# Optimization experiments

Measured on AMD Instinct MI355X. Metric: run time of the kernel, lower is better.

Reference implementation:

```python
import jax, jax.numpy as jnp
import numpy as np


def setup_inputs() -> dict:
    key = jax.random.key(0)
    ks = jax.random.split(key, 7)
    B, C, H, W = 8, 1024, 64, 64
    heads, head_dim, red = 8, 128, 8
    s = 1.0 / np.sqrt(head_dim)
    return {
        "x": jax.random.normal(ks[0], (B, C, H, W), jnp.float32),
        "Wq": jax.random.normal(ks[1], (heads, red, head_dim), jnp.float32) * s,
        "bq": jax.random.normal(ks[2], (heads, red), jnp.float32) * s,
        "Wk": jax.random.normal(ks[3], (heads, red, head_dim), jnp.float32) * s,
        "bk": jax.random.normal(ks[4], (heads, red), jnp.float32) * s,
        "Wv": jax.random.normal(ks[5], (heads, head_dim, head_dim), jnp.float32) * s,
        "bv": jax.random.normal(ks[6], (heads, head_dim), jnp.float32) * s,
    }


def reference(x, Wq, bq, Wk, bk, Wv, bv):
    B, C, H, W = x.shape
    heads, red, d = Wq.shape  # d = head_dim
    # (B, heads, head_dim, HW)
    xh = x.reshape(B, heads, d, H * W)
    # per-head spatial average pool: (B, heads, head_dim)
    avg = jnp.mean(xh, axis=-1)
    # torch Linear: y = x @ W.T + b, applied per head
    q = jnp.einsum("bhds,hrd->bhsr", xh, Wq) + bq[None, :, None, :]   # (B,H,S,r)
    k = jnp.einsum("bhd,hrd->bhr", avg, Wk) + bk[None]                 # (B,H,r)
    v = jnp.einsum("bhd,hed->bhe", avg, Wv) + bv[None]                 # (B,H,d)
    # single-key attention; softmax over the spatial dim (torch dim=1)
    scores = jnp.einsum("bhsr,bhr->bhs", q, k)                          # (B,H,S)
    attn = jax.nn.softmax(scores, axis=-1)
    out = jnp.einsum("bhs,bhe->bhes", attn, v)                          # (B,H,d,S)
    return out.reshape(B, C, H, W)
```

## Files before the change

### kernel.cpp

```cpp
#include <hip/hip_runtime.h>
#include <math.h>

#define SDIM 4096
#define DDIM 128
#define RED 8
#define BATCH 8
#define BH 64
#define CH 1024

typedef float vfloat4 __attribute__((ext_vector_type(4)));

#define WS_AVG  0
#define WS_VV   32768
#define WS_ATT  40960
#define WS_QRP  303104
#define QRP_DG  2097152

__inline__ __device__ float wave_reduce_sum(float v) {
#pragma unroll
    for (int o = 32; o > 0; o >>= 1) v += __shfl_down(v, o, 64);
    return v;
}
__inline__ __device__ float wave_reduce_max(float v) {
#pragma unroll
    for (int o = 32; o > 0; o >>= 1) v = fmaxf(v, __shfl_down(v, o, 64));
    return v;
}

__global__ __launch_bounds__(256, 4) void k_qr(
        const float* __restrict__ x, const float* __restrict__ Wq,
        float* __restrict__ ws) {
    const int blk = blockIdx.x;
    const int dg = blk & 3, chunk = (blk >> 2) & 3, bh = blk >> 4;
    const int h = bh & 7;
    const int t = threadIdx.x;
    const int wave = t >> 6, lane = t & 63;
    const int r8 = lane >> 3, seg = lane & 7;

    __shared__ float wqt[32 * 8];
    __shared__ float sxy[4][8][65];
    __shared__ float fpart[4][4][8][9];

    wqt[t] = Wq[(h * RED + (t & 7)) * DDIM + dg * 32 + (t >> 3)];
    __syncthreads();

    const int s0 = chunk * 1024 + t * 4;
    const float* xb = x + (size_t)(bh * DDIM + dg * 32) * SDIM + s0;
    vfloat4 accq[RED];
#pragma unroll
    for (int r = 0; r < RED; ++r) accq[r] = (vfloat4)0.f;

#pragma unroll
    for (int g = 0; g < 4; ++g) {
#pragma unroll
        for (int j = 0; j < 8; ++j) {
            const int dl = g * 8 + j;
            const vfloat4 xv = *(const vfloat4*)(xb + (size_t)dl * SDIM);
            const float4 wa = *(const float4*)&wqt[dl * 8];
            const float4 wb = *(const float4*)&wqt[dl * 8 + 4];
            accq[0] += xv * wa.x;
            accq[1] += xv * wa.y;
            accq[2] += xv * wa.z;
            accq[3] += xv * wa.w;
            accq[4] += xv * wb.x;
            accq[5] += xv * wb.y;
            accq[6] += xv * wb.z;
            accq[7] += xv * wb.w;
            sxy[wave][j][lane] = xv[0] + xv[1] + xv[2] + xv[3];
        }
        float ps = 0.f;
#pragma unroll
        for (int j = 0; j < 8; ++j) ps += sxy[wave][r8][seg * 8 + j];
        fpart[wave][g][r8][seg] = ps;
    }

    float* qb = ws + WS_QRP + (size_t)dg * QRP_DG + (size_t)(bh * RED) * SDIM + s0;
#pragma unroll
    for (int r = 0; r < RED; ++r)
        *(vfloat4*)(qb + (size_t)r * SDIM) = accq[r];

    __syncthreads();
    if (t < 32) {
        const int g = t >> 3, rr = t & 7;
        float a = 0.f;
#pragma unroll
        for (int w = 0; w < 4; ++w)
#pragma unroll
            for (int s2 = 0; s2 < 8; ++s2)
                a += fpart[w][g][rr][s2];
        ws[WS_AVG + chunk * 8192 + bh * DDIM + dg * 32 + t] = a;
    }
}

__global__ __launch_bounds__(256) void k_head(
        const float* __restrict__ bq, const float* __restrict__ Wk,
        const float* __restrict__ bk, const float* __restrict__ Wv,
        const float* __restrict__ bv, float* __restrict__ ws) {
    const int bh = blockIdx.x;
    const int h = bh & 7;
    const int t = threadIdx.x;
    const int wave = t >> 6, lane = t & 63;

    __shared__ float avgs[DDIM], kk[RED], bqs[RED];
    __shared__ float smax[4], ssum[4];
    __shared__ float cc;

    if (t < DDIM) {
        float a = 0.f;
#pragma unroll
        for (int c = 0; c < 4; ++c) a += ws[WS_AVG + c * 8192 + bh * DDIM + t];
        avgs[t] = a * (1.0f / SDIM);
    }
    __syncthreads();
    if (t < RED) {
        const float* wkr = Wk + (h * RED + t) * DDIM;
        float a = 0.f;
#pragma unroll 8
        for (int d = 0; d < DDIM; ++d) a += wkr[d] * avgs[d];
        kk[t] = a + bk[h * RED + t];
        bqs[t] = bq[h * RED + t];
    }
    if (t < DDIM) {
        const float* wvr = Wv + (h * DDIM + t) * DDIM;
        float a = 0.f;
#pragma unroll 8
        for (int d = 0; d < DDIM; ++d) a += wvr[d] * avgs[d];
        ws[WS_VV + bh * DDIM + t] = a + bv[h * DDIM + t];
    }
    __syncthreads();
    if (t == 0) {
        float a = 0.f;
#pragma unroll
        for (int r = 0; r < RED; ++r) a += bqs[r] * kk[r];
        cc = a;
    }
    __syncthreads();

    float4 vals[4];
    float m = -1e30f;
#pragma unroll
    for (int p = 0; p < 4; ++p) {
        float4 a;
        a.x = cc; a.y = cc; a.z = cc; a.w = cc;
#pragma unroll
        for (int r = 0; r < RED; ++r) {
            const size_t base = WS_QRP + (size_t)(bh * RED + r) * SDIM + (t + 256 * p) * 4;
            float4 q0 = *(const float4*)(ws + base);
            float4 q1 = *(const float4*)(ws + base + QRP_DG);
            float4 q2 = *(const float4*)(ws + base + 2 * (size_t)QRP_DG);
            float4 q3 = *(const float4*)(ws + base + 3 * (size_t)QRP_DG);
            const float kr = kk[r];
            a.x += (q0.x + q1.x + q2.x + q3.x) * kr;
            a.y += (q0.y + q1.y + q2.y + q3.y) * kr;
            a.z += (q0.z + q1.z + q2.z + q3.z) * kr;
            a.w += (q0.w + q1.w + q2.w + q3.w) * kr;
        }
        vals[p] = a;
        m = fmaxf(m, fmaxf(fmaxf(a.x, a.y), fmaxf(a.z, a.w)));
    }
    m = wave_reduce_max(m);
    if (lane == 0) smax[wave] = m;
    __syncthreads();
    const float gm = fmaxf(fmaxf(smax[0], smax[1]), fmaxf(smax[2], smax[3]));
    float sum = 0.f;
#pragma unroll
    for (int p = 0; p < 4; ++p) {
        vals[p].x = expf(vals[p].x - gm);
        vals[p].y = expf(vals[p].y - gm);
        vals[p].z = expf(vals[p].z - gm);
        vals[p].w = expf(vals[p].w - gm);
        sum += vals[p].x + vals[p].y + vals[p].z + vals[p].w;
    }
    sum = wave_reduce_sum(sum);
    if (lane == 0) ssum[wave] = sum;
    __syncthreads();
    const float inv = 1.0f / (ssum[0] + ssum[1] + ssum[2] + ssum[3]);
    float4* att4 = (float4*)(ws + WS_ATT + (size_t)bh * SDIM);
#pragma unroll
    for (int p = 0; p < 4; ++p) {
        float4 o;
        o.x = vals[p].x * inv; o.y = vals[p].y * inv;
        o.z = vals[p].z * inv; o.w = vals[p].w * inv;
        att4[t + 256 * p] = o;
    }
}

__global__ __launch_bounds__(256) void k_wr(const float* __restrict__ ws,
                                            float* __restrict__ out) {
    const int blk = blockIdx.x;
    const int bh = blk >> 4, chunk = blk & 15;
    const int t = threadIdx.x;
    const int wave = t >> 6, lane = t & 63;

    __shared__ float vvs[DDIM];
    if (t < DDIM) vvs[t] = ws[WS_VV + bh * DDIM + t];

    const vfloat4 a4 =
        ((const vfloat4*)(ws + WS_ATT))[bh * 1024 + chunk * 64 + lane];
    __syncthreads();

    vfloat4* ob = (vfloat4*)out + (size_t)(bh * DDIM) * 1024 + chunk * 64 + lane;
#pragma unroll
    for (int i = 0; i < 32; ++i) {
        const int e = wave * 32 + i;
        vfloat4 o = a4 * vvs[e];
        __builtin_nontemporal_store(o, ob + (size_t)e * 1024);
    }
}

extern "C" void kernel_launch(void* const* d_in, const int* in_sizes, int n_in,
                              void* d_out, int out_size, void* d_ws, size_t ws_size,
                              hipStream_t stream) {
    const float* x  = (const float*)d_in[0];
    const float* Wq = (const float*)d_in[1];
    const float* bq = (const float*)d_in[2];
    const float* Wk = (const float*)d_in[3];
    const float* bk = (const float*)d_in[4];
    const float* Wv = (const float*)d_in[5];
    const float* bv = (const float*)d_in[6];
    float* out = (float*)d_out;
    float* ws  = (float*)d_ws;

    k_qr<<<1024, 256, 0, stream>>>(x, Wq, ws);
    k_head<<<BH, 256, 0, stream>>>(bq, Wk, bk, Wv, bv, ws);
    k_wr<<<1024, 256, 0, stream>>>(ws, out);
}
```

Before: 276.3 us.

## Reduce full head_dim per block in q projection, drop partial-sum buffers

Each k_qr block now walks all 128 channels of a head over a 512-wide spatial chunk, using 128 threads, instead of splitting channels into four groups. This removes the four partial q buffers and the extra reads that summed them in k_head, cutting workspace traffic. In exchange the grid drops to 512 blocks of 128 threads with longer serial loops, which lowers parallelism and the latency hiding available for streaming x.

```diff
diff --git a/kernel.cpp b/kernel.cpp
--- a/kernel.cpp
+++ b/kernel.cpp
@@ -11,10 +11,9 @@
 typedef float vfloat4 __attribute__((ext_vector_type(4)));
 
 #define WS_AVG  0
-#define WS_VV   32768
-#define WS_ATT  40960
-#define WS_QRP  303104
-#define QRP_DG  2097152
+#define WS_VV   65536
+#define WS_ATT  73728
+#define WS_QR   335872
 
 __inline__ __device__ float wave_reduce_sum(float v) {
 #pragma unroll
@@ -27,37 +26,40 @@
     return v;
 }
 
-__global__ __launch_bounds__(256, 4) void k_qr(
+__global__ __launch_bounds__(128, 2) void k_qr(
         const float* __restrict__ x, const float* __restrict__ Wq,
         float* __restrict__ ws) {
     const int blk = blockIdx.x;
-    const int dg = blk & 3, chunk = (blk >> 2) & 3, bh = blk >> 4;
+    const int chunk = blk & 7, bh = blk >> 3;
     const int h = bh & 7;
     const int t = threadIdx.x;
     const int wave = t >> 6, lane = t & 63;
     const int r8 = lane >> 3, seg = lane & 7;
 
-    __shared__ float wqt[32 * 8];
-    __shared__ float sxy[4][8][65];
-    __shared__ float fpart[4][4][8][9];
-
-    wqt[t] = Wq[(h * RED + (t & 7)) * DDIM + dg * 32 + (t >> 3)];
-    __syncthreads();
-
-    const int s0 = chunk * 1024 + t * 4;
-    const float* xb = x + (size_t)(bh * DDIM + dg * 32) * SDIM + s0;
+    __shared__ float wqt[DDIM * RED];
+    __shared__ float sxy[2][8][65];
+    __shared__ float fpart[2][16][8][9];
+
+    for (int i = t; i < DDIM * RED; i += 128) {
+        const int d = i >> 3, r = i & 7;
+        wqt[i] = Wq[(h * RED + r) * DDIM + d];
+    }
+    __syncthreads();
+
+    const int s0 = chunk * 512 + t * 4;
+    const float* xb = x + (size_t)bh * DDIM * SDIM + s0;
     vfloat4 accq[RED];
 #pragma unroll
     for (int r = 0; r < RED; ++r) accq[r] = (vfloat4)0.f;
 
-#pragma unroll
-    for (int g = 0; g < 4; ++g) {
+#pragma unroll 2
+    for (int g = 0; g < 16; ++g) {
 #pragma unroll
         for (int j = 0; j < 8; ++j) {
-            const int dl = g * 8 + j;
-            const vfloat4 xv = *(const vfloat4*)(xb + (size_t)dl * SDIM);
-            const float4 wa = *(const float4*)&wqt[dl * 8];
-            const float4 wb = *(const float4*)&wqt[dl * 8 + 4];
+            const int d = g * 8 + j;
+            const vfloat4 xv = *(const vfloat4*)(xb + (size_t)d * SDIM);
+            const float4 wa = *(const float4*)&wqt[d * 8];
+            const float4 wb = *(const float4*)&wqt[d * 8 + 4];
             accq[0] += xv * wa.x;
             accq[1] += xv * wa.y;
             accq[2] += xv * wa.z;
@@ -74,21 +76,21 @@
         fpart[wave][g][r8][seg] = ps;
     }
 
-    float* qb = ws + WS_QRP + (size_t)dg * QRP_DG + (size_t)(bh * RED) * SDIM + s0;
+    float* qb = ws + WS_QR + (size_t)(bh * RED) * SDIM + s0;
 #pragma unroll
     for (int r = 0; r < RED; ++r)
         *(vfloat4*)(qb + (size_t)r * SDIM) = accq[r];
 
     __syncthreads();
-    if (t < 32) {
+    {
         const int g = t >> 3, rr = t & 7;
         float a = 0.f;
 #pragma unroll
-        for (int w = 0; w < 4; ++w)
+        for (int w = 0; w < 2; ++w)
 #pragma unroll
             for (int s2 = 0; s2 < 8; ++s2)
                 a += fpart[w][g][rr][s2];
-        ws[WS_AVG + chunk * 8192 + bh * DDIM + dg * 32 + t] = a;
+        ws[WS_AVG + chunk * 8192 + bh * DDIM + t] = a;
     }
 }
 
@@ -108,7 +110,7 @@
     if (t < DDIM) {
         float a = 0.f;
 #pragma unroll
-        for (int c = 0; c < 4; ++c) a += ws[WS_AVG + c * 8192 + bh * DDIM + t];
+        for (int c = 0; c < 8; ++c) a += ws[WS_AVG + c * 8192 + bh * DDIM + t];
         avgs[t] = a * (1.0f / SDIM);
     }
     __syncthreads();
@@ -136,6 +138,7 @@
     }
     __syncthreads();
 
+    const float4* qr4 = (const float4*)(ws + WS_QR + (size_t)(bh * RED) * SDIM);
     float4 vals[4];
     float m = -1e30f;
 #pragma unroll
@@ -144,16 +147,9 @@
         a.x = cc; a.y = cc; a.z = cc; a.w = cc;
 #pragma unroll
         for (int r = 0; r < RED; ++r) {
-            const size_t base = WS_QRP + (size_t)(bh * RED + r) * SDIM + (t + 256 * p) * 4;
-            float4 q0 = *(const float4*)(ws + base);
-            float4 q1 = *(const float4*)(ws + base + QRP_DG);
-            float4 q2 = *(const float4*)(ws + base + 2 * (size_t)QRP_DG);
-            float4 q3 = *(const float4*)(ws + base + 3 * (size_t)QRP_DG);
+            const float4 q = qr4[r * 1024 + t + 256 * p];
             const float kr = kk[r];
-            a.x += (q0.x + q1.x + q2.x + q3.x) * kr;
-            a.y += (q0.y + q1.y + q2.y + q3.y) * kr;
-            a.z += (q0.z + q1.z + q2.z + q3.z) * kr;
-            a.w += (q0.w + q1.w + q2.w + q3.w) * kr;
+            a.x += q.x * kr; a.y += q.y * kr; a.z += q.z * kr; a.w += q.w * kr;
         }
         vals[p] = a;
         m = fmaxf(m, fmaxf(fmaxf(a.x, a.y), fmaxf(a.z, a.w)));
@@ -214,14 +210,14 @@
     const float* x  = (const float*)d_in[0];
     const float* Wq = (const float*)d_in[1];
     const float* bq = (const float*)d_in[2];
+    const float* bk = (const float*)d_in[4];
     const float* Wk = (const float*)d_in[3];
-    const float* bk = (const float*)d_in[4];
     const float* Wv = (const float*)d_in[5];
     const float* bv = (const float*)d_in[6];
     float* out = (float*)d_out;
     float* ws  = (float*)d_ws;
 
-    k_qr<<<1024, 256, 0, stream>>>(x, Wq, ws);
+    k_qr<<<512, 128, 0, stream>>>(x, Wq, ws);
     k_head<<<BH, 256, 0, stream>>>(bq, Wk, bk, Wv, bv, ws);
     k_wr<<<1024, 256, 0, stream>>>(ws, out);
 }
```

New measurement: 298.2 us. 7.9% more time.
